# Kernel tuning notes

Measured on AMD Instinct MI355X. Metric: run time of the kernel, lower is better.

## Reference

```python
import jax, jax.numpy as jnp
import numpy as np

NUM_TREES = 256
DEPTH = 6
BATCH = 4096
FEATURES = 256


def setup_inputs() -> dict:
    key = jax.random.key(0)
    k1, k2, k3 = jax.random.split(key, 3)
    inputs = jax.random.normal(k1, (BATCH, FEATURES), dtype=jnp.float32)
    # Keras 'random_normal' initializer: stddev 0.05
    decision_weights = 0.05 * jax.random.normal(k2, (NUM_TREES, DEPTH, FEATURES), dtype=jnp.float32)
    thresholds = jnp.zeros((NUM_TREES, DEPTH), dtype=jnp.float32)
    leaf_weights = 0.05 * jax.random.normal(k3, (NUM_TREES, 2 ** DEPTH), dtype=jnp.float32)
    return {
        'inputs': inputs,
        'decision_weights': decision_weights,
        'thresholds': thresholds,
        'leaf_weights': leaf_weights,
    }


def reference(inputs, decision_weights, thresholds, leaf_weights):
    # Faithful to tf.einsum('bj,tdk->btd'): j and k are NOT shared, so both
    # are independently summed -> outer product of per-row sum and per-(t,d) sum.
    decisions = jnp.einsum('bj,tdk->btd', inputs, decision_weights)  # [B,T,D]
    decisions = jax.nn.sigmoid(decisions + thresholds)
    B = inputs.shape[0]
    T = decision_weights.shape[0]
    depth = decision_weights.shape[1]
    paths = jnp.ones((B, T, 1), dtype=inputs.dtype)
    for d in range(depth):  # loop over small fixed depth (structural)
        dl = decisions[:, :, d:d + 1]  # [B,T,1]
        paths = jnp.concatenate([paths * dl, paths * (1.0 - dl)], axis=2)
    outputs = jnp.einsum('btl,tl->bt', paths, leaf_weights)  # [B,T]
    return jnp.mean(outputs, axis=1, keepdims=True)  # [B,1]
```

## Files before the change

### kernel.cpp

```cpp
#include <hip/hip_runtime.h>
#include <hip/hip_bf16.h>


#define NUM_TREES 256
#define DEPTH 6
#define LEAVES 64
#define BATCH 4096
#define FEATURES 256
#define BPB 8

#define WS_SIN  0
#define WS_SWT  4096
#define WS_THT  5632
#define WS_B5   7168
#define WS_D5   15360

__global__ __launch_bounds__(256) void prep_kernel(
    const float* __restrict__ inputs,
    const float* __restrict__ dw,
    const float* __restrict__ thr,
    const float* __restrict__ leaf,
    float* __restrict__ ws)
{
    const int gw   = (blockIdx.x * blockDim.x + threadIdx.x) >> 6;
    const int lane = threadIdx.x & 63;
    const float scale = 1.0f / (float)NUM_TREES;

    if (gw < BATCH + NUM_TREES * DEPTH) {
        const float* src;
        float* dst;
        if (gw < BATCH) {
            src = inputs + (size_t)gw * FEATURES;
            dst = ws + WS_SIN + gw;
        } else {
            const int r = gw - BATCH;
            const int t = r / DEPTH;
            const int d = r - t * DEPTH;
            src = dw + (size_t)r * FEATURES;
            dst = ws + WS_SWT + d * NUM_TREES + t;
        }
        float4 v = reinterpret_cast<const float4*>(src)[lane];
        float s = (v.x + v.y) + (v.z + v.w);
#pragma unroll
        for (int off = 32; off > 0; off >>= 1)
            s += __shfl_down(s, off);
        if (lane == 0) *dst = s;
    } else if (gw < BATCH + NUM_TREES * DEPTH + 64) {
        const int j = gw - (BATCH + NUM_TREES * DEPTH);
        const int c = j >> 2;
        const int t = ((j & 3) << 6) | lane;
        const float4* lp = reinterpret_cast<const float4*>(leaf);
        if (c < 8) {
            float4 va = lp[t * (LEAVES / 4) + c];
            float4 vb = lp[t * (LEAVES / 4) + c + 8];
            float4 d;
            d.x = (va.x - vb.x) * scale; d.y = (va.y - vb.y) * scale;
            d.z = (va.z - vb.z) * scale; d.w = (va.w - vb.w) * scale;
            reinterpret_cast<float4*>(ws + WS_D5)[c * NUM_TREES + t] = d;
        } else {
            float4 vb = lp[t * (LEAVES / 4) + c];
            float4 b;
            b.x = vb.x * scale; b.y = vb.y * scale;
            b.z = vb.z * scale; b.w = vb.w * scale;
            reinterpret_cast<float4*>(ws + WS_B5)[(c - 8) * NUM_TREES + t] = b;
        }
    } else {
        const int j = gw - (BATCH + NUM_TREES * DEPTH + 64);
        const int idx = j * 64 + lane;
        const int t = idx / DEPTH;
        const int d = idx - t * DEPTH;
        ws[WS_THT + d * NUM_TREES + t] = thr[idx];
    }
}

__global__ __launch_bounds__(256, 1) void forest_kernel(
    const float* __restrict__ ws,
    float* __restrict__ out)
{
    const int t  = threadIdx.x;
    const int b0 = blockIdx.x * BPB;

    float sw[DEPTH], th[DEPTH];
#pragma unroll
    for (int d = 0; d < DEPTH; ++d) {
        sw[d] = ws[WS_SWT + d * NUM_TREES + t];
        th[d] = ws[WS_THT + d * NUM_TREES + t];
    }
    float b5[32], d5[32];
#pragma unroll
    for (int c = 0; c < 8; ++c) {
        float4 vb = reinterpret_cast<const float4*>(ws + WS_B5)[c * NUM_TREES + t];
        float4 vd = reinterpret_cast<const float4*>(ws + WS_D5)[c * NUM_TREES + t];
        b5[4 * c + 0] = vb.x; b5[4 * c + 1] = vb.y;
        b5[4 * c + 2] = vb.z; b5[4 * c + 3] = vb.w;
        d5[4 * c + 0] = vd.x; d5[4 * c + 1] = vd.y;
        d5[4 * c + 2] = vd.z; d5[4 * c + 3] = vd.w;
    }

    float res[BPB];
#pragma unroll
    for (int bi = 0; bi < BPB; ++bi) {
        const float si = ws[WS_SIN + b0 + bi];
        float dec[DEPTH];
#pragma unroll
        for (int d = 0; d < DEPTH; ++d) {
            const float x = fmaf(si, sw[d], th[d]);
            dec[d] = 1.0f / (1.0f + __expf(-x));
        }
        float m[32];
#pragma unroll
        for (int i = 0; i < 32; ++i) m[i] = fmaf(dec[5], d5[i], b5[i]);
#pragma unroll
        for (int i = 0; i < 16; ++i) m[i] = fmaf(dec[4], m[i] - m[i + 16], m[i + 16]);
#pragma unroll
        for (int i = 0; i < 8; ++i)  m[i] = fmaf(dec[3], m[i] - m[i + 8],  m[i + 8]);
#pragma unroll
        for (int i = 0; i < 4; ++i)  m[i] = fmaf(dec[2], m[i] - m[i + 4],  m[i + 4]);
#pragma unroll
        for (int i = 0; i < 2; ++i)  m[i] = fmaf(dec[1], m[i] - m[i + 2],  m[i + 2]);
        res[bi] = fmaf(dec[0], m[0] - m[1], m[1]);
    }

    __shared__ float red[4][BPB];
    const int lane = t & 63;
    const int wv   = t >> 6;
#pragma unroll
    for (int bi = 0; bi < BPB; ++bi) {
        float v = res[bi];
#pragma unroll
        for (int off = 32; off > 0; off >>= 1)
            v += __shfl_down(v, off);
        if (lane == 0) red[wv][bi] = v;
    }
    __syncthreads();
    if (t < BPB) {
        out[b0 + t] = red[0][t] + red[1][t] + red[2][t] + red[3][t];
    }
}

extern "C" void kernel_launch(void* const* d_in, const int* in_sizes, int n_in,
                              void* d_out, int out_size, void* d_ws, size_t ws_size,
                              hipStream_t stream) {
    const float* inputs = (const float*)d_in[0];
    const float* dw     = (const float*)d_in[1];
    const float* thr    = (const float*)d_in[2];
    const float* leaf   = (const float*)d_in[3];
    float* out = (float*)d_out;
    float* ws  = (float*)d_ws;

    prep_kernel<<<1430, 256, 0, stream>>>(inputs, dw, thr, leaf, ws);

    forest_kernel<<<BATCH / BPB, 256, 0, stream>>>(ws, out);
}
```

Before: 69.90 us.

## Fuse prep and forest kernels into one cooperative launch with grid sync

Merges the reduction/prep kernel and the forest evaluation kernel into a single cooperative kernel with 256 blocks. A grid-wide sync separates the phases, and each wave handles up to six row-sum reductions with all loads issued up front. BPB doubles to 16 so the grid fits co-resident. This removes the second kernel launch and the gap between launches, at the cost of grid-sync overhead and fewer blocks in the compute phase.

```diff
diff --git a/kernel.cpp b/kernel.cpp
--- a/kernel.cpp
+++ b/kernel.cpp
@@ -1,5 +1,7 @@
 #include <hip/hip_runtime.h>
-#include <hip/hip_bf16.h>
+#include <hip/hip_cooperative_groups.h>
+
+namespace cg = cooperative_groups;
 
 
 #define NUM_TREES 256
@@ -7,7 +9,10 @@
 #define LEAVES 64
 #define BATCH 4096
 #define FEATURES 256
-#define BPB 8
+#define BPB 16
+#define NBLK (BATCH / BPB)
+#define NWAVE (NBLK * 4)
+#define NROWS (BATCH + NUM_TREES * DEPTH)
 
 #define WS_SIN  0
 #define WS_SWT  4096
@@ -15,69 +20,86 @@
 #define WS_B5   7168
 #define WS_D5   15360
 
-__global__ __launch_bounds__(256) void prep_kernel(
+__global__ __launch_bounds__(256, 1) void fused_kernel(
     const float* __restrict__ inputs,
     const float* __restrict__ dw,
     const float* __restrict__ thr,
     const float* __restrict__ leaf,
-    float* __restrict__ ws)
+    float* __restrict__ ws,
+    float* __restrict__ out)
 {
-    const int gw   = (blockIdx.x * blockDim.x + threadIdx.x) >> 6;
-    const int lane = threadIdx.x & 63;
+    const int tid  = threadIdx.x;
+    const int lane = tid & 63;
+    const int wv   = tid >> 6;
+    const int wg   = blockIdx.x * 4 + wv;
     const float scale = 1.0f / (float)NUM_TREES;
 
-    if (gw < BATCH + NUM_TREES * DEPTH) {
-        const float* src;
-        float* dst;
-        if (gw < BATCH) {
-            src = inputs + (size_t)gw * FEATURES;
-            dst = ws + WS_SIN + gw;
-        } else {
-            const int r = gw - BATCH;
-            const int t = r / DEPTH;
-            const int d = r - t * DEPTH;
-            src = dw + (size_t)r * FEATURES;
-            dst = ws + WS_SWT + d * NUM_TREES + t;
-        }
-        float4 v = reinterpret_cast<const float4*>(src)[lane];
+    float4 va, vb;
+    float thval = 0.0f;
+    int lf_c = 0, lf_t = 0, th_idx = 0;
+    if (wg < 32) {
+        lf_c = wg >> 2;
+        lf_t = ((wg & 3) << 6) | lane;
+        const float4* lp = reinterpret_cast<const float4*>(leaf);
+        va = lp[lf_t * (LEAVES / 4) + lf_c];
+        vb = lp[lf_t * (LEAVES / 4) + lf_c + 8];
+    } else if (wg < 56) {
+        th_idx = (wg - 32) * 64 + lane;
+        thval = thr[th_idx];
+    }
+
+#define ROWPTR(task) ((task) < BATCH ? inputs + (size_t)(task) * FEATURES \
+                                     : dw + (size_t)((task) - BATCH) * FEATURES)
+    const float4 r0 = reinterpret_cast<const float4*>(ROWPTR(wg            ))[lane];
+    const float4 r1 = reinterpret_cast<const float4*>(ROWPTR(wg + 1 * NWAVE))[lane];
+    const float4 r2 = reinterpret_cast<const float4*>(ROWPTR(wg + 2 * NWAVE))[lane];
+    const float4 r3 = reinterpret_cast<const float4*>(ROWPTR(wg + 3 * NWAVE))[lane];
+    const float4 r4 = reinterpret_cast<const float4*>(ROWPTR(wg + 4 * NWAVE))[lane];
+    const bool has5 = (wg + 5 * NWAVE) < NROWS;
+    float4 r5;
+    if (has5) r5 = reinterpret_cast<const float4*>(ROWPTR(wg + 5 * NWAVE))[lane];
+
+    if (wg < 32) {
+        float4 d, b;
+        d.x = (va.x - vb.x) * scale; d.y = (va.y - vb.y) * scale;
+        d.z = (va.z - vb.z) * scale; d.w = (va.w - vb.w) * scale;
+        b.x = vb.x * scale; b.y = vb.y * scale;
+        b.z = vb.z * scale; b.w = vb.w * scale;
+        reinterpret_cast<float4*>(ws + WS_D5)[lf_c * NUM_TREES + lf_t] = d;
+        reinterpret_cast<float4*>(ws + WS_B5)[lf_c * NUM_TREES + lf_t] = b;
+    } else if (wg < 56) {
+        const int t = th_idx / DEPTH;
+        const int d = th_idx - t * DEPTH;
+        ws[WS_THT + d * NUM_TREES + t] = thval;
+    }
+
+    auto reduce_store = [&](float4 v, int task) {
         float s = (v.x + v.y) + (v.z + v.w);
 #pragma unroll
         for (int off = 32; off > 0; off >>= 1)
             s += __shfl_down(s, off);
-        if (lane == 0) *dst = s;
-    } else if (gw < BATCH + NUM_TREES * DEPTH + 64) {
-        const int j = gw - (BATCH + NUM_TREES * DEPTH);
-        const int c = j >> 2;
-        const int t = ((j & 3) << 6) | lane;
-        const float4* lp = reinterpret_cast<const float4*>(leaf);
-        if (c < 8) {
-            float4 va = lp[t * (LEAVES / 4) + c];
-            float4 vb = lp[t * (LEAVES / 4) + c + 8];
-            float4 d;
-            d.x = (va.x - vb.x) * scale; d.y = (va.y - vb.y) * scale;
-            d.z = (va.z - vb.z) * scale; d.w = (va.w - vb.w) * scale;
-            reinterpret_cast<float4*>(ws + WS_D5)[c * NUM_TREES + t] = d;
-        } else {
-            float4 vb = lp[t * (LEAVES / 4) + c];
-            float4 b;
-            b.x = vb.x * scale; b.y = vb.y * scale;
-            b.z = vb.z * scale; b.w = vb.w * scale;
-            reinterpret_cast<float4*>(ws + WS_B5)[(c - 8) * NUM_TREES + t] = b;
+        if (lane == 0) {
+            if (task < BATCH) {
+                ws[WS_SIN + task] = s;
+            } else {
+                const int r = task - BATCH;
+                const int t = r / DEPTH;
+                const int d = r - t * DEPTH;
+                ws[WS_SWT + d * NUM_TREES + t] = s;
+            }
         }
-    } else {
-        const int j = gw - (BATCH + NUM_TREES * DEPTH + 64);
-        const int idx = j * 64 + lane;
-        const int t = idx / DEPTH;
-        const int d = idx - t * DEPTH;
-        ws[WS_THT + d * NUM_TREES + t] = thr[idx];
-    }
-}
+    };
+    reduce_store(r0, wg);
+    reduce_store(r1, wg + 1 * NWAVE);
+    reduce_store(r2, wg + 2 * NWAVE);
+    reduce_store(r3, wg + 3 * NWAVE);
+    reduce_store(r4, wg + 4 * NWAVE);
+    if (has5) reduce_store(r5, wg + 5 * NWAVE);
 
-__global__ __launch_bounds__(256, 1) void forest_kernel(
-    const float* __restrict__ ws,
-    float* __restrict__ out)
-{
-    const int t  = threadIdx.x;
+    __threadfence();
+    cg::this_grid().sync();
+
+    const int t  = tid;
     const int b0 = blockIdx.x * BPB;
 
     float sw[DEPTH], th[DEPTH];
@@ -89,12 +111,12 @@
     float b5[32], d5[32];
 #pragma unroll
     for (int c = 0; c < 8; ++c) {
-        float4 vb = reinterpret_cast<const float4*>(ws + WS_B5)[c * NUM_TREES + t];
-        float4 vd = reinterpret_cast<const float4*>(ws + WS_D5)[c * NUM_TREES + t];
-        b5[4 * c + 0] = vb.x; b5[4 * c + 1] = vb.y;
-        b5[4 * c + 2] = vb.z; b5[4 * c + 3] = vb.w;
-        d5[4 * c + 0] = vd.x; d5[4 * c + 1] = vd.y;
-        d5[4 * c + 2] = vd.z; d5[4 * c + 3] = vd.w;
+        float4 vbv = reinterpret_cast<const float4*>(ws + WS_B5)[c * NUM_TREES + t];
+        float4 vdv = reinterpret_cast<const float4*>(ws + WS_D5)[c * NUM_TREES + t];
+        b5[4 * c + 0] = vbv.x; b5[4 * c + 1] = vbv.y;
+        b5[4 * c + 2] = vbv.z; b5[4 * c + 3] = vbv.w;
+        d5[4 * c + 0] = vdv.x; d5[4 * c + 1] = vdv.y;
+        d5[4 * c + 2] = vdv.z; d5[4 * c + 3] = vdv.w;
     }
 
     float res[BPB];
@@ -122,8 +144,6 @@
     }
 
     __shared__ float red[4][BPB];
-    const int lane = t & 63;
-    const int wv   = t >> 6;
 #pragma unroll
     for (int bi = 0; bi < BPB; ++bi) {
         float v = res[bi];
@@ -133,8 +153,8 @@
         if (lane == 0) red[wv][bi] = v;
     }
     __syncthreads();
-    if (t < BPB) {
-        out[b0 + t] = red[0][t] + red[1][t] + red[2][t] + red[3][t];
+    if (tid < BPB) {
+        out[b0 + tid] = red[0][tid] + red[1][tid] + red[2][tid] + red[3][tid];
     }
 }
 
@@ -148,7 +168,8 @@
     float* out = (float*)d_out;
     float* ws  = (float*)d_ws;
 
-    prep_kernel<<<1430, 256, 0, stream>>>(inputs, dw, thr, leaf, ws);
-
-    forest_kernel<<<BATCH / BPB, 256, 0, stream>>>(ws, out);
+    void* args[] = {(void*)&inputs, (void*)&dw, (void*)&thr, (void*)&leaf,
+                    (void*)&ws, (void*)&out};
+    hipLaunchCooperativeKernel((void*)fused_kernel, dim3(NBLK), dim3(256),
+                               args, 0, stream);
 }
```

After: 122.5 us. 1.75x slower.

## Fuse per-row input sums into forest kernel and use fast reciprocal

Applied to the files above, without the earlier changes.

Moves the per-row input reductions out of the prep kernel and into the forest kernel. Each wave now loads two input rows and reduces them with shuffles into shared memory, so the workspace round trip for row sums goes away and the prep grid shrinks. The sigmoid division is also replaced by the hardware reciprocal intrinsic. The cost is an extra barrier and input loads in the main kernel, plus slightly lower precision in the sigmoid.

```diff
diff --git a/kernel.cpp b/kernel.cpp
--- a/kernel.cpp
+++ b/kernel.cpp
@@ -9,14 +9,12 @@
 #define FEATURES 256
 #define BPB 8
 
-#define WS_SIN  0
-#define WS_SWT  4096
-#define WS_THT  5632
-#define WS_B5   7168
-#define WS_D5   15360
+#define WS_SWT  0
+#define WS_THT  1536
+#define WS_B5   3072
+#define WS_D5   11264
 
 __global__ __launch_bounds__(256) void prep_kernel(
-    const float* __restrict__ inputs,
     const float* __restrict__ dw,
     const float* __restrict__ thr,
     const float* __restrict__ leaf,
@@ -26,27 +24,17 @@
     const int lane = threadIdx.x & 63;
     const float scale = 1.0f / (float)NUM_TREES;
 
-    if (gw < BATCH + NUM_TREES * DEPTH) {
-        const float* src;
-        float* dst;
-        if (gw < BATCH) {
-            src = inputs + (size_t)gw * FEATURES;
-            dst = ws + WS_SIN + gw;
-        } else {
-            const int r = gw - BATCH;
-            const int t = r / DEPTH;
-            const int d = r - t * DEPTH;
-            src = dw + (size_t)r * FEATURES;
-            dst = ws + WS_SWT + d * NUM_TREES + t;
-        }
-        float4 v = reinterpret_cast<const float4*>(src)[lane];
+    if (gw < NUM_TREES * DEPTH) {
+        const int t = gw / DEPTH;
+        const int d = gw - t * DEPTH;
+        float4 v = reinterpret_cast<const float4*>(dw + (size_t)gw * FEATURES)[lane];
         float s = (v.x + v.y) + (v.z + v.w);
 #pragma unroll
         for (int off = 32; off > 0; off >>= 1)
             s += __shfl_down(s, off);
-        if (lane == 0) *dst = s;
-    } else if (gw < BATCH + NUM_TREES * DEPTH + 64) {
-        const int j = gw - (BATCH + NUM_TREES * DEPTH);
+        if (lane == 0) ws[WS_SWT + d * NUM_TREES + t] = s;
+    } else if (gw < NUM_TREES * DEPTH + 64) {
+        const int j = gw - NUM_TREES * DEPTH;
         const int c = j >> 2;
         const int t = ((j & 3) << 6) | lane;
         const float4* lp = reinterpret_cast<const float4*>(leaf);
@@ -65,7 +53,7 @@
             reinterpret_cast<float4*>(ws + WS_B5)[(c - 8) * NUM_TREES + t] = b;
         }
     } else {
-        const int j = gw - (BATCH + NUM_TREES * DEPTH + 64);
+        const int j = gw - (NUM_TREES * DEPTH + 64);
         const int idx = j * 64 + lane;
         const int t = idx / DEPTH;
         const int d = idx - t * DEPTH;
@@ -74,12 +62,20 @@
 }
 
 __global__ __launch_bounds__(256, 1) void forest_kernel(
+    const float* __restrict__ inputs,
     const float* __restrict__ ws,
     float* __restrict__ out)
 {
-    const int t  = threadIdx.x;
-    const int b0 = blockIdx.x * BPB;
+    const int tid  = threadIdx.x;
+    const int lane = tid & 63;
+    const int wv   = tid >> 6;
+    const int b0   = blockIdx.x * BPB;
 
+    const float4* ip = reinterpret_cast<const float4*>(inputs);
+    const float4 a0 = ip[(size_t)(b0 + 2 * wv)     * (FEATURES / 4) + lane];
+    const float4 a1 = ip[(size_t)(b0 + 2 * wv + 1) * (FEATURES / 4) + lane];
+
+    const int t = tid;
     float sw[DEPTH], th[DEPTH];
 #pragma unroll
     for (int d = 0; d < DEPTH; ++d) {
@@ -97,15 +93,26 @@
         d5[4 * c + 2] = vd.z; d5[4 * c + 3] = vd.w;
     }
 
+    float s0 = (a0.x + a0.y) + (a0.z + a0.w);
+    float s1 = (a1.x + a1.y) + (a1.z + a1.w);
+#pragma unroll
+    for (int off = 32; off > 0; off >>= 1) {
+        s0 += __shfl_down(s0, off);
+        s1 += __shfl_down(s1, off);
+    }
+    __shared__ float sib[BPB];
+    if (lane == 0) { sib[2 * wv] = s0; sib[2 * wv + 1] = s1; }
+    __syncthreads();
+
     float res[BPB];
 #pragma unroll
     for (int bi = 0; bi < BPB; ++bi) {
-        const float si = ws[WS_SIN + b0 + bi];
+        const float si = sib[bi];
         float dec[DEPTH];
 #pragma unroll
         for (int d = 0; d < DEPTH; ++d) {
             const float x = fmaf(si, sw[d], th[d]);
-            dec[d] = 1.0f / (1.0f + __expf(-x));
+            dec[d] = __builtin_amdgcn_rcpf(1.0f + __expf(-x));
         }
         float m[32];
 #pragma unroll
@@ -122,8 +129,6 @@
     }
 
     __shared__ float red[4][BPB];
-    const int lane = t & 63;
-    const int wv   = t >> 6;
 #pragma unroll
     for (int bi = 0; bi < BPB; ++bi) {
         float v = res[bi];
@@ -133,8 +138,8 @@
         if (lane == 0) red[wv][bi] = v;
     }
     __syncthreads();
-    if (t < BPB) {
-        out[b0 + t] = red[0][t] + red[1][t] + red[2][t] + red[3][t];
+    if (tid < BPB) {
+        out[b0 + tid] = red[0][tid] + red[1][tid] + red[2][tid] + red[3][tid];
     }
 }
 
@@ -148,7 +153,7 @@
     float* out = (float*)d_out;
     float* ws  = (float*)d_ws;
 
-    prep_kernel<<<1430, 256, 0, stream>>>(inputs, dw, thr, leaf, ws);
+    prep_kernel<<<406, 256, 0, stream>>>(dw, thr, leaf, ws);
 
-    forest_kernel<<<BATCH / BPB, 256, 0, stream>>>(ws, out);
+    forest_kernel<<<BATCH / BPB, 256, 0, stream>>>(inputs, ws, out);
 }
```

Measured after the change: 68.89 us. No clear change (-1.4%).
